# Kernel tuning notes

Measured on AMD Instinct MI355X. Metric: run time of the kernel, lower is better.

The kernel has to match this reference:

```python
import jax, jax.numpy as jnp
import numpy as np

DIM = 512
QK_DIM = 128
HIDDEN = 2 * DIM  # expansion_factor * dim
EPS = 1e-5


def layernorm(x, scale, bias):
    mu = jnp.mean(x, axis=-1, keepdims=True)
    var = jnp.mean((x - mu) ** 2, axis=-1, keepdims=True)
    return (x - mu) * jax.lax.rsqrt(var + EPS) * scale + bias


def setup_inputs() -> dict:
    key = jax.random.key(0)
    ks = jax.random.split(key, 8)
    b, s = 4, 4096
    x = jax.random.normal(ks[0], (b, s, DIM), dtype=jnp.float32)
    inv = lambda fan_in: 1.0 / np.sqrt(fan_in)
    W_hidden = jax.random.normal(ks[1], (DIM, 2 * HIDDEN), dtype=jnp.float32) * inv(DIM)
    b_hidden = jnp.zeros((2 * HIDDEN,), dtype=jnp.float32)
    W_qk = jax.random.normal(ks[2], (DIM, QK_DIM), dtype=jnp.float32) * inv(DIM)
    b_qk = jnp.zeros((QK_DIM,), dtype=jnp.float32)
    gamma = jax.random.normal(ks[3], (2, QK_DIM), dtype=jnp.float32) * 0.02
    beta = jnp.zeros((2, QK_DIM), dtype=jnp.float32)
    W_out = jax.random.normal(ks[4], (HIDDEN, DIM), dtype=jnp.float32) * inv(HIDDEN)
    b_out = jnp.zeros((DIM,), dtype=jnp.float32)
    norm_scale = jnp.ones((DIM,), dtype=jnp.float32)
    norm_bias = jnp.zeros((DIM,), dtype=jnp.float32)
    return {
        "x": x,
        "norm_scale": norm_scale,
        "norm_bias": norm_bias,
        "W_hidden": W_hidden,
        "b_hidden": b_hidden,
        "W_qk": W_qk,
        "b_qk": b_qk,
        "gamma": gamma,
        "beta": beta,
        "W_out": W_out,
        "b_out": b_out,
    }


def reference(x, norm_scale, norm_bias, W_hidden, b_hidden, W_qk, b_qk, gamma, beta, W_out, b_out):
    seq_len = x.shape[-2]
    normed = layernorm(x, norm_scale, norm_bias)
    hidden = jax.nn.silu(normed @ W_hidden + b_hidden)          # [b, s, 2*hidden]
    v, gate = jnp.split(hidden, 2, axis=-1)                      # each [b, s, hidden]
    Z = jax.nn.silu(normed @ W_qk + b_qk)                        # [b, s, qk]
    QK = Z[..., None, :] * gamma + beta                          # [b, s, 2, qk]
    q = QK[..., 0, :]
    k = QK[..., 1, :]
    sim = jnp.einsum('bid,bjd->bij', q, k) / seq_len             # [b, s, s]
    A = jnp.square(jax.nn.relu(sim))
    V = jnp.einsum('bij,bjd->bid', A, v) * gate                  # [b, s, hidden]
    out = V @ W_out + b_out
    return out + x
```

## Files before the change

### kernel.cpp

```cpp
#include <hip/hip_runtime.h>
#include <cstdint>
#include <cstddef>

#define DIM   512
#define QKD   128
#define HID   1024
#define SEQ   4096
#define BAT   4
#define TOK   (BAT*SEQ)

typedef float f32x4 __attribute__((ext_vector_type(4)));
typedef int   i32x4 __attribute__((ext_vector_type(4)));
typedef int   i32x8 __attribute__((ext_vector_type(8)));

__device__ __forceinline__ float silu_f(float x) { return x / (1.f + __expf(-x)); }

__device__ __forceinline__ unsigned char f2e4(float f) {
    int v = __builtin_amdgcn_cvt_pk_fp8_f32(f, 0.f, 0, false);
    return (unsigned char)(v & 0xff);
}
__device__ __forceinline__ unsigned f2e4x4(float a, float b, float c, float d) {
    int w = __builtin_amdgcn_cvt_pk_fp8_f32(a, b, 0, false);
    w = __builtin_amdgcn_cvt_pk_fp8_f32(c, d, w, true);
    return (unsigned)w;
}
__device__ __forceinline__ float e42f(unsigned char b) {
    return __builtin_amdgcn_cvt_f32_fp8((int)b, 0);
}

__device__ __forceinline__ void load16_lds(const void* gp, void* lp) {
    __builtin_amdgcn_global_load_lds(
        (const __attribute__((address_space(1))) unsigned int*)gp,
        (__attribute__((address_space(3))) unsigned int*)lp,
        16, 0, 0);
}

__global__ __launch_bounds__(256) void ln_kernel(
    const float* __restrict__ x, const float* __restrict__ sc,
    const float* __restrict__ bi, unsigned char* __restrict__ out)
{
    const int lane = threadIdx.x & 63, wid = threadIdx.x >> 6;
    const int row  = blockIdx.x * 4 + wid;
    const float4* xr = (const float4*)(x + (size_t)row * DIM);
    float4 a = xr[lane], b = xr[64 + lane];
    float s = a.x + a.y + a.z + a.w + b.x + b.y + b.z + b.w;
    float q = a.x*a.x + a.y*a.y + a.z*a.z + a.w*a.w
            + b.x*b.x + b.y*b.y + b.z*b.z + b.w*b.w;
#pragma unroll
    for (int m = 1; m < 64; m <<= 1) { s += __shfl_xor(s, m); q += __shfl_xor(q, m); }
    const float mean = s * (1.f / DIM);
    const float var  = q * (1.f / DIM) - mean * mean;
    const float rs   = rsqrtf(var + 1e-5f);
    float4 s0 = ((const float4*)sc)[lane], s1 = ((const float4*)sc)[64 + lane];
    float4 b0 = ((const float4*)bi)[lane], b1 = ((const float4*)bi)[64 + lane];
    unsigned wlo = f2e4x4((a.x - mean) * rs * s0.x + b0.x,
                          (a.y - mean) * rs * s0.y + b0.y,
                          (a.z - mean) * rs * s0.z + b0.z,
                          (a.w - mean) * rs * s0.w + b0.w);
    unsigned whi = f2e4x4((b.x - mean) * rs * s1.x + b1.x,
                          (b.y - mean) * rs * s1.y + b1.y,
                          (b.z - mean) * rs * s1.z + b1.z,
                          (b.w - mean) * rs * s1.w + b1.w);
    unsigned char* orow = out + (size_t)row * DIM;
    *(unsigned*)(orow + 4 * lane)       = wlo;
    *(unsigned*)(orow + 256 + 4 * lane) = whi;
}

__global__ __launch_bounds__(256) void tcast_f2e4_kernel(
    const float* __restrict__ in, unsigned char* __restrict__ out, int R, int C)
{
    __shared__ float t[32][33];
    const int tx = threadIdx.x & 31, ty = threadIdx.x >> 5;
    const int c0 = blockIdx.x * 32, r0 = blockIdx.y * 32;
#pragma unroll
    for (int i = 0; i < 4; ++i)
        t[ty + i * 8][tx] = in[(size_t)(r0 + ty + i * 8) * C + c0 + tx];
    __syncthreads();
#pragma unroll
    for (int i = 0; i < 4; ++i)
        out[(size_t)(c0 + ty + i * 8) * R + r0 + tx] = f2e4(t[tx][ty + i * 8] * 16.f);
}

__global__ __launch_bounds__(256) void copy_kernel(
    const float* __restrict__ in, float* __restrict__ out, int n4)
{
    int i = blockIdx.x * 256 + threadIdx.x;
    int stride = gridDim.x * 256;
    for (; i < n4; i += stride)
        ((float4*)out)[i] = ((const float4*)in)[i];
}

template<int EPI, int NX>
__global__ __launch_bounds__(256) void gemm8(
    const unsigned char* __restrict__ A, const unsigned char* __restrict__ B,
    int K, long strAz, long strBz, long strOz,
    const float* __restrict__ f0, const float* __restrict__ f1,
    const float* __restrict__ f2, const float* __restrict__ f3,
    const float* __restrict__ f4, const float* __restrict__ f5,
    unsigned char* __restrict__ gate,
    unsigned char* __restrict__ o0, unsigned char* __restrict__ o1,
    unsigned char* __restrict__ o2,
    float* __restrict__ fo, float scale)
{
    __shared__ unsigned char lds[32768];
    const int tid = threadIdx.x;
    const int d  = blockIdx.x + NX * blockIdx.y;
    const int qd = d >> 3;
    const int m0 = ((d & 7) + 8 * (qd / NX)) * 128;
    const int n0 = (qd % NX) * 128;
    const int z  = blockIdx.z;
    A += (size_t)z * strAz;  B += (size_t)z * strBz;
    const int lane = tid & 63, wid = tid >> 6;
    const int wm   = (wid & 1) * 64, wn = (wid >> 1) * 64;
    const int l15  = lane & 15, quad = lane >> 4;

    f32x4 acc[4][4] = {};

    const int srow = tid >> 3, sseg = tid & 7;
    const int gseg = sseg ^ (srow & 7);
    const unsigned char* gA = A + (size_t)(m0 + srow) * K + gseg * 16;
    const unsigned char* gB = B + (size_t)(n0 + srow) * K + gseg * 16;
    unsigned char* lA = lds + (size_t)tid * 16;
    unsigned char* lB = lds + 16384 + (size_t)tid * 16;

    const int olo = (((quad << 1) ^ (l15 & 7)) << 4);
    const int ohi = olo ^ 16;

    for (int kt = 0; kt < K; kt += 128) {
#pragma unroll
        for (int i = 0; i < 4; ++i)
            load16_lds(gA + (size_t)i * 32 * K + kt, lA + i * 4096);
#pragma unroll
        for (int i = 0; i < 4; ++i)
            load16_lds(gB + (size_t)i * 32 * K + kt, lB + i * 4096);
        __syncthreads();
        i32x4 alo[4], ahi[4], blo[4], bhi[4];
#pragma unroll
        for (int mi = 0; mi < 4; ++mi) {
            const unsigned char* p = lds + (wm + mi * 16 + l15) * 128;
            alo[mi] = *(const i32x4*)(p + olo); ahi[mi] = *(const i32x4*)(p + ohi);
        }
#pragma unroll
        for (int ni = 0; ni < 4; ++ni) {
            const unsigned char* p = lds + 16384 + (wn + ni * 16 + l15) * 128;
            blo[ni] = *(const i32x4*)(p + olo); bhi[ni] = *(const i32x4*)(p + ohi);
        }
#pragma unroll
        for (int mi = 0; mi < 4; ++mi) {
            i32x8 af = __builtin_shufflevector(alo[mi], ahi[mi], 0,1,2,3,4,5,6,7);
#pragma unroll
            for (int ni = 0; ni < 4; ++ni) {
                i32x8 bf = __builtin_shufflevector(blo[ni], bhi[ni], 0,1,2,3,4,5,6,7);
                acc[mi][ni] = __builtin_amdgcn_mfma_scale_f32_16x16x128_f8f6f4(
                    af, bf, acc[mi][ni], 0, 0,
                    0, 0x7F7F7F7F, 0, 0x7F7F7F7F);
            }
        }
        __syncthreads();
    }

#pragma unroll
    for (int mi = 0; mi < 4; ++mi)
#pragma unroll
    for (int ni = 0; ni < 4; ++ni) {
        const int grow0 = m0 + wm + mi * 16 + quad * 4;
        const int gcol  = n0 + wn + ni * 16 + l15;
        if constexpr (EPI == 0) {
            if (gcol < HID) {
                const int b = grow0 >> 12, rloc = grow0 & (SEQ - 1);
                unsigned w = f2e4x4(silu_f(acc[mi][ni][0] * 0.0625f + f0[gcol]),
                                    silu_f(acc[mi][ni][1] * 0.0625f + f0[gcol]),
                                    silu_f(acc[mi][ni][2] * 0.0625f + f0[gcol]),
                                    silu_f(acc[mi][ni][3] * 0.0625f + f0[gcol]));
                *(unsigned*)(o0 + (size_t)b * HID * SEQ + (size_t)gcol * SEQ + rloc) = w;
            } else if (gcol < 2048) {
#pragma unroll
                for (int r = 0; r < 4; ++r)
                    gate[(size_t)(grow0 + r) * HID + (gcol - HID)] =
                        f2e4(silu_f(acc[mi][ni][r] * 0.0625f + f0[gcol]));
            } else {
                const int c = gcol - 2048;
#pragma unroll
                for (int r = 0; r < 4; ++r) {
                    float zf = silu_f(acc[mi][ni][r] * 0.0625f + f1[c]);
                    o1[(size_t)(grow0 + r) * QKD + c] = f2e4((zf * f2[c] + f4[c]) * 64.f);
                    o2[(size_t)(grow0 + r) * QKD + c] = f2e4((zf * f3[c] + f5[c]) * 64.f);
                }
            }
        } else if constexpr (EPI == 1) {
            unsigned char* Ao = o0 + (size_t)z * strOz;
#pragma unroll
            for (int r = 0; r < 4; ++r) {
                float t = fmaxf(acc[mi][ni][r], 0.f) * 0.0625f;
                Ao[(size_t)(grow0 + r) * SEQ + gcol] = f2e4(t * t);
            }
        } else if constexpr (EPI == 2) {
            unsigned char* gz = gate + (size_t)z * strOz;
            unsigned char* vo = o0 + (size_t)z * strOz;
#pragma unroll
            for (int r = 0; r < 4; ++r) {
                float g = e42f(gz[(size_t)(grow0 + r) * HID + gcol]);
                vo[(size_t)(grow0 + r) * HID + gcol] = f2e4(acc[mi][ni][r] * scale * g);
            }
        } else {
#pragma unroll
            for (int r = 0; r < 4; ++r)
                fo[(size_t)(grow0 + r) * DIM + gcol] =
                    acc[mi][ni][r] * scale + f0[gcol] + f1[(size_t)(grow0 + r) * DIM + gcol];
        }
    }
}

extern "C" void kernel_launch(void* const* d_in, const int* in_sizes, int n_in,
                              void* d_out, int out_size, void* d_ws, size_t ws_size,
                              hipStream_t stream) {
    const float* x     = (const float*)d_in[0];
    const float* nsc   = (const float*)d_in[1];
    const float* nbi   = (const float*)d_in[2];
    const float* Wh    = (const float*)d_in[3];
    const float* bh    = (const float*)d_in[4];
    const float* Wqk   = (const float*)d_in[5];
    const float* bqk   = (const float*)d_in[6];
    const float* gamma = (const float*)d_in[7];
    const float* beta  = (const float*)d_in[8];
    const float* Wout  = (const float*)d_in[9];
    const float* bout  = (const float*)d_in[10];
    float* out = (float*)d_out;

    uint8_t* ws = (uint8_t*)d_ws;
    size_t off = 0;
    auto alloc = [&](size_t n) { uint8_t* p = ws + off; off += (n + 255) & ~(size_t)255; return p; };
    unsigned char* normed8 = (unsigned char*)alloc((size_t)TOK * DIM);
    unsigned char* Wc8     = (unsigned char*)alloc((size_t)2176 * DIM);
    unsigned char* Wout8   = (unsigned char*)alloc((size_t)DIM * HID);
    unsigned char* vT8     = (unsigned char*)alloc((size_t)BAT * HID * SEQ);
    unsigned char* gbuf    = (unsigned char*)alloc((size_t)TOK * HID);
    unsigned char* q8      = (unsigned char*)alloc((size_t)TOK * QKD);
    unsigned char* k8      = (unsigned char*)alloc((size_t)TOK * QKD);
    unsigned char* Ab8     = (unsigned char*)alloc((size_t)BAT * SEQ * SEQ);
    unsigned char* vg8     = (unsigned char*)alloc((size_t)TOK * HID);

    if (ws_size < off) {
        copy_kernel<<<4096, 256, 0, stream>>>(x, out, TOK * DIM / 4);
        return;
    }

    ln_kernel<<<TOK / 4, 256, 0, stream>>>(x, nsc, nbi, normed8);
    tcast_f2e4_kernel<<<dim3(2048 / 32, DIM / 32), 256, 0, stream>>>(Wh, Wc8, DIM, 2048);
    tcast_f2e4_kernel<<<dim3(QKD / 32, DIM / 32), 256, 0, stream>>>(
        Wqk, Wc8 + (size_t)2048 * DIM, DIM, QKD);
    tcast_f2e4_kernel<<<dim3(DIM / 32, HID / 32), 256, 0, stream>>>(Wout, Wout8, HID, DIM);

    gemm8<0, 17><<<dim3(17, TOK / 128), 256, 0, stream>>>(
        normed8, Wc8, DIM, 0, 0, 0,
        bh, bqk, gamma, gamma + QKD, beta, beta + QKD,
        gbuf, vT8, q8, k8, nullptr, 0.f);

    gemm8<1, 32><<<dim3(SEQ / 128, SEQ / 128, BAT), 256, 0, stream>>>(
        q8, k8, QKD, (long)SEQ * QKD, (long)SEQ * QKD, (long)SEQ * SEQ,
        nullptr, nullptr, nullptr, nullptr, nullptr, nullptr,
        nullptr, Ab8, nullptr, nullptr, nullptr, 0.f);

    gemm8<2, 8><<<dim3(HID / 128, SEQ / 128, BAT), 256, 0, stream>>>(
        Ab8, vT8, SEQ, (long)SEQ * SEQ, (long)HID * SEQ, (long)SEQ * HID,
        nullptr, nullptr, nullptr, nullptr, nullptr, nullptr,
        gbuf, vg8, nullptr, nullptr, nullptr, 0x1p-12f);

    gemm8<3, 4><<<dim3(DIM / 128, TOK / 128), 256, 0, stream>>>(
        vg8, Wout8, HID, 0, 0, 0,
        bout, x, nullptr, nullptr, nullptr, nullptr,
        nullptr, nullptr, nullptr, nullptr, out, 0x1p-32f);
}
```

Measured before the change: 286.9 us.

## Add triple-buffered 256x128 GEMM kernel with explicit vmcnt waits

Adds a new gemm8p kernel that uses 512 threads and a 256-row by 128-column tile. It triple-buffers LDS with async global-to-LDS loads, waits on the memory counter with explicit vmcnt instructions, and issues one barrier per K-step so loads overlap compute. The hidden projection, the A·V GEMM and the output projection now use this kernel, while QK^T keeps the old gemm8. The cost is about 144KB of LDS per block, which limits occupancy, and the hand-placed waitcnt logic is fragile.

```diff
diff --git a/kernel.cpp b/kernel.cpp
--- a/kernel.cpp
+++ b/kernel.cpp
@@ -34,6 +34,10 @@
         (__attribute__((address_space(3))) unsigned int*)lp,
         16, 0, 0);
 }
+
+#define WAITV6() asm volatile("s_waitcnt vmcnt(6)" ::: "memory")
+#define WAITV0() asm volatile("s_waitcnt vmcnt(0)" ::: "memory")
+#define FENCE()  do { asm volatile("" ::: "memory"); __builtin_amdgcn_sched_barrier(0); } while (0)
 
 __global__ __launch_bounds__(256) void ln_kernel(
     const float* __restrict__ x, const float* __restrict__ sc,
@@ -165,6 +169,116 @@
     for (int ni = 0; ni < 4; ++ni) {
         const int grow0 = m0 + wm + mi * 16 + quad * 4;
         const int gcol  = n0 + wn + ni * 16 + l15;
+        if constexpr (EPI == 1) {
+            unsigned char* Ao = o0 + (size_t)z * strOz;
+#pragma unroll
+            for (int r = 0; r < 4; ++r) {
+                float t = fmaxf(acc[mi][ni][r], 0.f) * 0.0625f;
+                Ao[(size_t)(grow0 + r) * SEQ + gcol] = f2e4(t * t);
+            }
+        }
+    }
+}
+
+template<int EPI, int NX>
+__global__ __launch_bounds__(512, 2) void gemm8p(
+    const unsigned char* __restrict__ A, const unsigned char* __restrict__ B,
+    int K, long strAz, long strBz, long strOz,
+    const float* __restrict__ f0, const float* __restrict__ f1,
+    const float* __restrict__ f2, const float* __restrict__ f3,
+    const float* __restrict__ f4, const float* __restrict__ f5,
+    unsigned char* __restrict__ gate,
+    unsigned char* __restrict__ o0, unsigned char* __restrict__ o1,
+    unsigned char* __restrict__ o2,
+    float* __restrict__ fo, float scale)
+{
+    __shared__ unsigned char lds[3 * 49152];
+    const int tid = threadIdx.x;
+    const int d  = blockIdx.x + NX * blockIdx.y;
+    const int qd = d >> 3;
+    const int m0 = ((d & 7) + 8 * (qd / NX)) * 256;
+    const int n0 = (qd % NX) * 128;
+    const int z  = blockIdx.z;
+    A += (size_t)z * strAz;  B += (size_t)z * strBz;
+    const int lane = tid & 63, wid = tid >> 6;
+    const int wm   = (wid & 3) * 64, wn = (wid >> 2) * 64;
+    const int l15  = lane & 15, quad = lane >> 4;
+
+    f32x4 acc[4][4] = {};
+
+    const int srow = tid >> 3, sseg = tid & 7;
+    const int gseg = sseg ^ (srow & 7);
+    const unsigned char* gAs = A + (size_t)(m0 + srow) * K + gseg * 16;
+    const unsigned char* gBs = B + (size_t)(n0 + srow) * K + gseg * 16;
+
+    const int olo = (((quad << 1) ^ (l15 & 7)) << 4);
+    const int ohi = olo ^ 16;
+
+    const int NT = K >> 7;
+
+    auto STAGE = [&](int t, int buf) {
+        const size_t ko = (size_t)t << 7;
+        unsigned char* lb = lds + buf * 49152 + tid * 16;
+#pragma unroll
+        for (int i = 0; i < 4; ++i)
+            load16_lds(gAs + (size_t)(i * 64) * K + ko, lb + i * 8192);
+#pragma unroll
+        for (int i = 0; i < 2; ++i)
+            load16_lds(gBs + (size_t)(i * 64) * K + ko, lb + 32768 + i * 8192);
+    };
+
+    auto COMPUTE = [&](int buf) {
+        const unsigned char* la = lds + buf * 49152;
+        const unsigned char* lb = la + 32768;
+        i32x4 alo[4], ahi[4], blo[4], bhi[4];
+#pragma unroll
+        for (int mi = 0; mi < 4; ++mi) {
+            const unsigned char* p = la + (size_t)(wm + mi * 16 + l15) * 128;
+            alo[mi] = *(const i32x4*)(p + olo); ahi[mi] = *(const i32x4*)(p + ohi);
+        }
+#pragma unroll
+        for (int ni = 0; ni < 4; ++ni) {
+            const unsigned char* p = lb + (size_t)(wn + ni * 16 + l15) * 128;
+            blo[ni] = *(const i32x4*)(p + olo); bhi[ni] = *(const i32x4*)(p + ohi);
+        }
+#pragma unroll
+        for (int mi = 0; mi < 4; ++mi) {
+            i32x8 af = __builtin_shufflevector(alo[mi], ahi[mi], 0,1,2,3,4,5,6,7);
+#pragma unroll
+            for (int ni = 0; ni < 4; ++ni) {
+                i32x8 bf = __builtin_shufflevector(blo[ni], bhi[ni], 0,1,2,3,4,5,6,7);
+                acc[mi][ni] = __builtin_amdgcn_mfma_scale_f32_16x16x128_f8f6f4(
+                    af, bf, acc[mi][ni], 0, 0,
+                    0, 0x7F7F7F7F, 0, 0x7F7F7F7F);
+            }
+        }
+    };
+
+    STAGE(0, 0);
+    if (NT > 1) { STAGE(1, 1); WAITV6(); }
+    else        {              WAITV0(); }
+    __builtin_amdgcn_s_barrier();
+    FENCE();
+
+    int cbuf = 0, sbuf = 2;
+    for (int t = 0; t < NT; ++t) {
+        if (t + 2 < NT) STAGE(t + 2, sbuf);
+        COMPUTE(cbuf);
+        if (t + 1 < NT) {
+            if (t + 2 < NT) WAITV6(); else WAITV0();
+            __builtin_amdgcn_s_barrier();
+            FENCE();
+        }
+        cbuf = (cbuf == 2) ? 0 : cbuf + 1;
+        sbuf = (sbuf == 2) ? 0 : sbuf + 1;
+    }
+
+#pragma unroll
+    for (int mi = 0; mi < 4; ++mi)
+#pragma unroll
+    for (int ni = 0; ni < 4; ++ni) {
+        const int grow0 = m0 + wm + mi * 16 + quad * 4;
+        const int gcol  = n0 + wn + ni * 16 + l15;
         if constexpr (EPI == 0) {
             if (gcol < HID) {
                 const int b = grow0 >> 12, rloc = grow0 & (SEQ - 1);
@@ -251,7 +365,7 @@
         Wqk, Wc8 + (size_t)2048 * DIM, DIM, QKD);
     tcast_f2e4_kernel<<<dim3(DIM / 32, HID / 32), 256, 0, stream>>>(Wout, Wout8, HID, DIM);
 
-    gemm8<0, 17><<<dim3(17, TOK / 128), 256, 0, stream>>>(
+    gemm8p<0, 17><<<dim3(17, TOK / 256), 512, 0, stream>>>(
         normed8, Wc8, DIM, 0, 0, 0,
         bh, bqk, gamma, gamma + QKD, beta, beta + QKD,
         gbuf, vT8, q8, k8, nullptr, 0.f);
@@ -261,12 +375,12 @@
         nullptr, nullptr, nullptr, nullptr, nullptr, nullptr,
         nullptr, Ab8, nullptr, nullptr, nullptr, 0.f);
 
-    gemm8<2, 8><<<dim3(HID / 128, SEQ / 128, BAT), 256, 0, stream>>>(
+    gemm8p<2, 8><<<dim3(HID / 128, SEQ / 256, BAT), 512, 0, stream>>>(
         Ab8, vT8, SEQ, (long)SEQ * SEQ, (long)HID * SEQ, (long)SEQ * HID,
         nullptr, nullptr, nullptr, nullptr, nullptr, nullptr,
         gbuf, vg8, nullptr, nullptr, nullptr, 0x1p-12f);
 
-    gemm8<3, 4><<<dim3(DIM / 128, TOK / 128), 256, 0, stream>>>(
+    gemm8p<3, 4><<<dim3(DIM / 128, TOK / 256), 512, 0, stream>>>(
         vg8, Wout8, HID, 0, 0, 0,
         bout, x, nullptr, nullptr, nullptr, nullptr,
         nullptr, nullptr, nullptr, nullptr, out, 0x1p-32f);
```

Measured after the change: 280.9 us (median of 2 runs). 1.02x faster.
